# Kernel optimization log

Measured on AMD Instinct MI355X. Metric: run time of the kernel, lower is better.

## Reference

```python
import jax, jax.numpy as jnp
import numpy as np

HIDDEN = 1024
STATE = 16
EXPAND = 2
INNER = HIDDEN * EXPAND
BATCH, SEQ = 4, 2048


def setup_inputs() -> dict:
    key = jax.random.key(0)
    ks = jax.random.split(key, 12)
    s = 0.02
    return {
        "x": jax.random.normal(ks[0], (BATCH, SEQ, HIDDEN), jnp.float32),
        "norm_scale": jnp.ones((HIDDEN,), jnp.float32),
        "norm_bias": jnp.zeros((HIDDEN,), jnp.float32),
        "W_in": jax.random.normal(ks[1], (HIDDEN, 2 * INNER), jnp.float32) * s,
        "conv_w": jax.random.normal(ks[2], (INNER, 3), jnp.float32) * 0.3,
        "conv_b": jnp.zeros((INNER,), jnp.float32),
        "W_dt": jax.random.normal(ks[3], (INNER, INNER), jnp.float32) * s,
        "b_dt": jnp.zeros((INNER,), jnp.float32),
        "A_log": jax.random.normal(ks[4], (INNER, STATE), jnp.float32),
        "D_param": jnp.ones((INNER,), jnp.float32),
        "W_B": jax.random.normal(ks[5], (INNER, STATE), jnp.float32) * s,
        "W_C": jax.random.normal(ks[6], (INNER, STATE), jnp.float32) * s,
        "W_out": jax.random.normal(ks[7], (INNER, HIDDEN), jnp.float32) * s,
    }


def reference(x, norm_scale, norm_bias, W_in, conv_w, conv_b, W_dt, b_dt,
              A_log, D_param, W_B, W_C, W_out):
    residual = x
    # LayerNorm (eps = 1e-5, matches nn.LayerNorm default)
    mu = jnp.mean(x, axis=-1, keepdims=True)
    var = jnp.mean(jnp.square(x - mu), axis=-1, keepdims=True)
    xn = (x - mu) * jax.lax.rsqrt(var + 1e-5) * norm_scale + norm_bias

    xz = xn @ W_in                         # [B, L, 2*inner]
    xb, z = jnp.split(xz, 2, axis=-1)      # each [B, L, inner]

    # depthwise conv1d, kernel 3, padding 1 (cross-correlation as in torch)
    xp = jnp.pad(xb, ((0, 0), (1, 1), (0, 0)))
    xb = (conv_w[:, 0] * xp[:, :-2] + conv_w[:, 1] * xp[:, 1:-1]
          + conv_w[:, 2] * xp[:, 2:] + conv_b)
    xb = jax.nn.silu(xb)

    dt = jax.nn.softplus(xb @ W_dt + b_dt)  # [B, L, inner]
    A = -jnp.exp(A_log)                     # [inner, N]
    Bi = xb @ W_B                           # [B, L, N]
    Ci = xb @ W_C                           # [B, L, N]

    def step(h, inp):
        x_t, dt_t, B_t, C_t = inp           # [B,D], [B,D], [B,N], [B,N]
        A_bar = jnp.exp(dt_t[:, :, None] * A)                 # [B, D, N]
        h = A_bar * h + (dt_t * x_t)[:, :, None] * B_t[:, None, :]
        y_t = jnp.einsum('bdn,bn->bd', h, C_t)
        return h, y_t

    h0 = jnp.zeros((x.shape[0], INNER, STATE), x.dtype)
    xs = (jnp.swapaxes(xb, 0, 1), jnp.swapaxes(dt, 0, 1),
          jnp.swapaxes(Bi, 0, 1), jnp.swapaxes(Ci, 0, 1))
    _, y = jax.lax.scan(step, h0, xs)       # y: [L, B, D]
    y = jnp.swapaxes(y, 0, 1)

    y = (y + D_param * xb) * jax.nn.silu(z)
    return residual + y @ W_out
```

## Files before the change

kernel.cpp:

```cpp
#include <hip/hip_runtime.h>
#include <hip/hip_bf16.h>
#include <cstdint>
#include <cstddef>

#define B_DIM 4
#define L_DIM 2048
#define H_DIM 1024
#define D_DIM 2048
#define N_STATE 16
#define TOKENS (B_DIM * L_DIM)
#define CH 16
#define LC (L_DIM / CH)
#define NEXT 2176

typedef __bf16 bf16x8 __attribute__((ext_vector_type(8)));
typedef float f32x4 __attribute__((ext_vector_type(4)));

__device__ __forceinline__ float sigmoidf_(float x) { return 1.f / (1.f + __expf(-x)); }
__device__ __forceinline__ float softplusf_(float x) {
  return fmaxf(x, 0.f) + log1pf(__expf(-fabsf(x)));
}
__device__ __forceinline__ void gl_lds16(const void* g, void* l) {
  __builtin_amdgcn_global_load_lds(
      (const __attribute__((address_space(1))) unsigned int*)g,
      (__attribute__((address_space(3))) unsigned int*)l, 16, 0, 0);
}

__global__ __launch_bounds__(256) void ln_kernel(const float* __restrict__ x,
    const float* __restrict__ gamma, const float* __restrict__ beta,
    __hip_bfloat16* __restrict__ out) {
  int row = blockIdx.x;
  int t = threadIdx.x;
  const float* px = x + (size_t)row * H_DIM;
  float4 v = *(const float4*)(px + t * 4);
  float s  = v.x + v.y + v.z + v.w;
  float ss = v.x * v.x + v.y * v.y + v.z * v.z + v.w * v.w;
  for (int off = 32; off > 0; off >>= 1) {
    s  += __shfl_down(s, off);
    ss += __shfl_down(ss, off);
  }
  __shared__ float red[8];
  __shared__ float stats[2];
  int wave = t >> 6, lane = t & 63;
  if (lane == 0) { red[wave] = s; red[4 + wave] = ss; }
  __syncthreads();
  if (t == 0) {
    float S  = red[0] + red[1] + red[2] + red[3];
    float SS = red[4] + red[5] + red[6] + red[7];
    float mu = S / H_DIM;
    float var = SS / H_DIM - mu * mu;
    stats[0] = mu;
    stats[1] = rsqrtf(var + 1e-5f);
  }
  __syncthreads();
  float mu = stats[0], rstd = stats[1];
  float4 g  = *(const float4*)(gamma + t * 4);
  float4 bt = *(const float4*)(beta + t * 4);
  __hip_bfloat16* po = out + (size_t)row * H_DIM + t * 4;
  po[0] = __float2bfloat16((v.x - mu) * rstd * g.x + bt.x);
  po[1] = __float2bfloat16((v.y - mu) * rstd * g.y + bt.y);
  po[2] = __float2bfloat16((v.z - mu) * rstd * g.z + bt.z);
  po[3] = __float2bfloat16((v.w - mu) * rstd * g.w + bt.w);
}

__global__ void transpose_bf16(const float* __restrict__ in,
                               __hip_bfloat16* __restrict__ out, int R, int C) {
  __shared__ float tile[32][33];
  int c0 = blockIdx.x * 32, r0 = blockIdx.y * 32;
  int tx = threadIdx.x, ty = threadIdx.y;
  for (int i = 0; i < 32; i += 8)
    tile[ty + i][tx] = in[(size_t)(r0 + ty + i) * C + c0 + tx];
  __syncthreads();
  for (int i = 0; i < 32; i += 8)
    out[(size_t)(c0 + ty + i) * R + r0 + tx] = __float2bfloat16(tile[tx][ty + i]);
}

__global__ __launch_bounds__(256) void wbc_transpose(const float* __restrict__ WB,
    const float* __restrict__ WC, __hip_bfloat16* __restrict__ Wext) {
  int tid = blockIdx.x * 256 + threadIdx.x;
  int c = tid & 31;
  int k0 = (tid >> 5) * 16;
  const float* W = (c < 16) ? WB : WC;
  int cc = c & 15;
  __hip_bfloat16* o = Wext + (size_t)(2048 + c) * D_DIM + k0;
  for (int kk = 0; kk < 16; ++kk)
    o[kk] = __float2bfloat16(W[(size_t)(k0 + kk) * N_STATE + cc]);
}

#define BM 128
#define BN 128
#define BK 64

template <int MODE>
__global__ __launch_bounds__(256) void gemm_bf16(
    const __hip_bfloat16* __restrict__ A, const __hip_bfloat16* __restrict__ Bt,
    void* __restrict__ C0, void* __restrict__ C1, int nsplit,
    int K, int lda, int ldb, int ldc, int gx,
    const float* __restrict__ bias, const float* __restrict__ resid) {
  __shared__ __hip_bfloat16 As[BM * BK];
  __shared__ __hip_bfloat16 Bs[BN * BK];
  int t = threadIdx.x;
  int bid = blockIdx.x;
  int nsup = gx << 3;
  int super = bid / nsup;
  int rem = bid - super * nsup;
  int m0 = (super * 8 + (rem & 7)) * BM;
  int n0 = (rem >> 3) * BN;

  int wave = t >> 6, lane = t & 63;
  int quad = lane >> 4, l16 = lane & 15;
  int wm = (wave >> 1) * 64, wn = (wave & 1) * 64;

  f32x4 acc[4][4] = {};

  int srow  = t >> 3;
  int cslot = t & 7;
  int cdata = cslot ^ (srow & 7);
  const __hip_bfloat16* Ag[4];
  const __hip_bfloat16* Bg[4];
  __hip_bfloat16* Asl[4];
  __hip_bfloat16* Bsl[4];
#pragma unroll
  for (int j = 0; j < 4; ++j) {
    Ag[j]  = A  + (size_t)(m0 + j * 32 + srow) * lda + cdata * 8;
    Bg[j]  = Bt + (size_t)(n0 + j * 32 + srow) * ldb + cdata * 8;
    Asl[j] = &As[(j * 32 + srow) * BK + cslot * 8];
    Bsl[j] = &Bs[(j * 32 + srow) * BK + cslot * 8];
  }

  for (int k0 = 0; k0 < K; k0 += BK) {
    __syncthreads();
#pragma unroll
    for (int j = 0; j < 4; ++j) {
      gl_lds16(Ag[j] + k0, Asl[j]);
      gl_lds16(Bg[j] + k0, Bsl[j]);
    }
    __syncthreads();
#pragma unroll
    for (int s = 0; s < 2; ++s) {
      int cs = ((s * 4 + quad) ^ (l16 & 7)) * 8;
      bf16x8 af[4], bf_[4];
#pragma unroll
      for (int i = 0; i < 4; ++i) {
        af[i]  = *(const bf16x8*)&As[(wm + i * 16 + l16) * BK + cs];
        bf_[i] = *(const bf16x8*)&Bs[(wn + i * 16 + l16) * BK + cs];
      }
#pragma unroll
      for (int i = 0; i < 4; ++i)
#pragma unroll
        for (int j = 0; j < 4; ++j)
          acc[i][j] = __builtin_amdgcn_mfma_f32_16x16x32_bf16(af[i], bf_[j], acc[i][j], 0, 0, 0);
    }
  }

#pragma unroll
  for (int i = 0; i < 4; ++i) {
    int row0 = m0 + wm + i * 16 + quad * 4;
#pragma unroll
    for (int j = 0; j < 4; ++j) {
      int col = n0 + wn + j * 16 + l16;
      f32x4 v = acc[i][j];
      if (MODE == 0) {
#pragma unroll
        for (int r = 0; r < 4; ++r) {
          size_t idx = (size_t)(row0 + r) * ldc + col;
          ((float*)C0)[idx] = v[r] + resid[idx];
        }
      } else if (MODE == 1) {
        bool mainc = (col < nsplit);
        __hip_bfloat16* cb = mainc ? (__hip_bfloat16*)C0 : (__hip_bfloat16*)C1;
        int ccol = mainc ? col : col - nsplit;
#pragma unroll
        for (int r = 0; r < 4; ++r)
          cb[(size_t)(row0 + r) * ldc + ccol] = __float2bfloat16(v[r]);
      } else {
        if (col < nsplit) {
          float bb = bias[col];
#pragma unroll
          for (int r = 0; r < 4; ++r)
            ((__hip_bfloat16*)C0)[(size_t)(row0 + r) * ldc + col] =
                __float2bfloat16(softplusf_(v[r] + bb));
        } else {
#pragma unroll
          for (int r = 0; r < 4; ++r)
            ((float*)C1)[(size_t)(row0 + r) * 128 + (col - nsplit)] = v[r];
        }
      }
    }
  }
}

__global__ __launch_bounds__(256) void conv_silu_kernel(const __hip_bfloat16* __restrict__ xb,
    const float* __restrict__ cw, const float* __restrict__ cb,
    __hip_bfloat16* __restrict__ xbc) {
  size_t i2 = (size_t)blockIdx.x * 256 + threadIdx.x;
  int dp = (int)(i2 & (D_DIM / 2 - 1));
  size_t tok = i2 >> 10;
  int l = (int)(tok & (L_DIM - 1));
  int d = dp * 2;
  const __hip_bfloat162* base = (const __hip_bfloat162*)xb + i2;
  __hip_bfloat162 cc = base[0];
  float v0 = cw[d * 3 + 1] * __bfloat162float(cc.x) + cb[d];
  float v1 = cw[d * 3 + 4] * __bfloat162float(cc.y) + cb[d + 1];
  if (l > 0) {
    __hip_bfloat162 pm = base[-(D_DIM / 2)];
    v0 += cw[d * 3 + 0] * __bfloat162float(pm.x);
    v1 += cw[d * 3 + 3] * __bfloat162float(pm.y);
  }
  if (l < L_DIM - 1) {
    __hip_bfloat162 pp = base[D_DIM / 2];
    v0 += cw[d * 3 + 2] * __bfloat162float(pp.x);
    v1 += cw[d * 3 + 5] * __bfloat162float(pp.y);
  }
  v0 = v0 * sigmoidf_(v0);
  v1 = v1 * sigmoidf_(v1);
  __hip_bfloat162 o;
  o.x = __float2bfloat16(v0);
  o.y = __float2bfloat16(v1);
  ((__hip_bfloat162*)xbc)[i2] = o;
}

__global__ __launch_bounds__(256) void scan1_kernel(const __hip_bfloat16* __restrict__ dt,
    const __hip_bfloat16* __restrict__ xbc, const float* __restrict__ BiCi,
    const float* __restrict__ A_log, float* __restrict__ hfin,
    float* __restrict__ dtsum) {
  __shared__ float Bsh[LC * N_STATE];
  int t = threadIdx.x;
  int d = blockIdx.x * 256 + t;
  int c = blockIdx.y, b = blockIdx.z;
  size_t base = (size_t)b * L_DIM + (size_t)c * LC;
  for (int idx = t; idx < LC * 4; idx += 256) {
    int row = idx >> 2, q = idx & 3;
    ((float4*)Bsh)[row * 4 + q] = *(const float4*)&BiCi[(base + row) * 128 + q * 4];
  }
  float Aneg[N_STATE];
  {
    const float4* Ap = (const float4*)(A_log + (size_t)d * N_STATE);
#pragma unroll
    for (int q = 0; q < 4; ++q) {
      float4 av = Ap[q];
      Aneg[4 * q + 0] = -__expf(av.x);
      Aneg[4 * q + 1] = -__expf(av.y);
      Aneg[4 * q + 2] = -__expf(av.z);
      Aneg[4 * q + 3] = -__expf(av.w);
    }
  }
  __syncthreads();
  const __hip_bfloat16* dtp = dt + base * D_DIM + d;
  const __hip_bfloat16* xp = xbc + base * D_DIM + d;
  float h[N_STATE];
#pragma unroll
  for (int n = 0; n < N_STATE; ++n) h[n] = 0.f;
  float ds = 0.f;
  float dtv = __bfloat162float(dtp[0]), xv = __bfloat162float(xp[0]);
  for (int i = 0; i < LC; ++i) {
    int ip = (i < LC - 1) ? i + 1 : i;
    float dt2 = __bfloat162float(dtp[(size_t)ip * D_DIM]);
    float x2  = __bfloat162float(xp[(size_t)ip * D_DIM]);
    float dtx = dtv * xv;
    ds += dtv;
    const float4* Brow = (const float4*)&Bsh[i * N_STATE];
#pragma unroll
    for (int q = 0; q < 4; ++q) {
      float4 bv = Brow[q];
      h[4*q+0] = __expf(dtv * Aneg[4*q+0]) * h[4*q+0] + dtx * bv.x;
      h[4*q+1] = __expf(dtv * Aneg[4*q+1]) * h[4*q+1] + dtx * bv.y;
      h[4*q+2] = __expf(dtv * Aneg[4*q+2]) * h[4*q+2] + dtx * bv.z;
      h[4*q+3] = __expf(dtv * Aneg[4*q+3]) * h[4*q+3] + dtx * bv.w;
    }
    dtv = dt2; xv = x2;
  }
  float* ho = hfin + (((size_t)b * CH + c) * D_DIM + d) * N_STATE;
#pragma unroll
  for (int q = 0; q < 4; ++q) {
    float4 v; v.x = h[4*q]; v.y = h[4*q+1]; v.z = h[4*q+2]; v.w = h[4*q+3];
    ((float4*)ho)[q] = v;
  }
  dtsum[((size_t)b * CH + c) * D_DIM + d] = ds;
}

__global__ __launch_bounds__(256) void scan2_kernel(const float* __restrict__ hfin,
    const float* __restrict__ dtsum, const float* __restrict__ A_log,
    float* __restrict__ hstart) {
  int tid = blockIdx.x * 256 + threadIdx.x;
  int n = tid & 15;
  int d = (tid >> 4) & (D_DIM - 1);
  int b = tid >> 15;
  float Aneg = -__expf(A_log[d * N_STATE + n]);
  float run = 0.f;
  for (int c = 0; c < CH; ++c) {
    size_t o = (((size_t)b * CH + c) * D_DIM + d) * N_STATE + n;
    hstart[o] = run;
    run = __expf(Aneg * dtsum[((size_t)b * CH + c) * D_DIM + d]) * run + hfin[o];
  }
}

__global__ __launch_bounds__(256) void scan3_kernel(const __hip_bfloat16* __restrict__ dt,
    const __hip_bfloat16* __restrict__ xbc, const float* __restrict__ BiCi,
    const float* __restrict__ A_log,
    const float* __restrict__ hstart, const __hip_bfloat16* __restrict__ z,
    const float* __restrict__ Dp, __hip_bfloat16* __restrict__ yo) {
  __shared__ float Bsh[LC * N_STATE];
  __shared__ float Csh[LC * N_STATE];
  int t = threadIdx.x;
  int d = blockIdx.x * 256 + t;
  int c = blockIdx.y, b = blockIdx.z;
  size_t base = (size_t)b * L_DIM + (size_t)c * LC;
  for (int idx = t; idx < LC * 4; idx += 256) {
    int row = idx >> 2, q = idx & 3;
    ((float4*)Bsh)[row * 4 + q] = *(const float4*)&BiCi[(base + row) * 128 + q * 4];
    ((float4*)Csh)[row * 4 + q] = *(const float4*)&BiCi[(base + row) * 128 + 16 + q * 4];
  }
  float Aneg[N_STATE];
  {
    const float4* Ap = (const float4*)(A_log + (size_t)d * N_STATE);
#pragma unroll
    for (int q = 0; q < 4; ++q) {
      float4 av = Ap[q];
      Aneg[4 * q + 0] = -__expf(av.x);
      Aneg[4 * q + 1] = -__expf(av.y);
      Aneg[4 * q + 2] = -__expf(av.z);
      Aneg[4 * q + 3] = -__expf(av.w);
    }
  }
  float h[N_STATE];
  {
    const float4* hs = (const float4*)(hstart + (((size_t)b * CH + c) * D_DIM + d) * N_STATE);
#pragma unroll
    for (int q = 0; q < 4; ++q) {
      float4 v = hs[q];
      h[4*q] = v.x; h[4*q+1] = v.y; h[4*q+2] = v.z; h[4*q+3] = v.w;
    }
  }
  float Dv = Dp[d];
  __syncthreads();
  const __hip_bfloat16* dtp = dt + base * D_DIM + d;
  const __hip_bfloat16* xp = xbc + base * D_DIM + d;
  const __hip_bfloat16* zp = z + base * D_DIM + d;
  __hip_bfloat16* yp = yo + base * D_DIM + d;
  float dtv = __bfloat162float(dtp[0]), xv = __bfloat162float(xp[0]);
  float zv = __bfloat162float(zp[0]);
  for (int i = 0; i < LC; ++i) {
    int ip = (i < LC - 1) ? i + 1 : i;
    float dt2 = __bfloat162float(dtp[(size_t)ip * D_DIM]);
    float x2  = __bfloat162float(xp[(size_t)ip * D_DIM]);
    float z2  = __bfloat162float(zp[(size_t)ip * D_DIM]);
    float dtx = dtv * xv;
    const float4* Brow = (const float4*)&Bsh[i * N_STATE];
    const float4* Crow = (const float4*)&Csh[i * N_STATE];
    float yv = 0.f;
#pragma unroll
    for (int q = 0; q < 4; ++q) {
      float4 bv = Brow[q];
      float4 cv = Crow[q];
      h[4*q+0] = __expf(dtv * Aneg[4*q+0]) * h[4*q+0] + dtx * bv.x;
      h[4*q+1] = __expf(dtv * Aneg[4*q+1]) * h[4*q+1] + dtx * bv.y;
      h[4*q+2] = __expf(dtv * Aneg[4*q+2]) * h[4*q+2] + dtx * bv.z;
      h[4*q+3] = __expf(dtv * Aneg[4*q+3]) * h[4*q+3] + dtx * bv.w;
      yv += h[4*q+0] * cv.x + h[4*q+1] * cv.y + h[4*q+2] * cv.z + h[4*q+3] * cv.w;
    }
    float g = zv * sigmoidf_(zv);
    yp[(size_t)i * D_DIM] = __float2bfloat16((yv + Dv * xv) * g);
    dtv = dt2; xv = x2; zv = z2;
  }
}

extern "C" void kernel_launch(void* const* d_in, const int* in_sizes, int n_in,
                              void* d_out, int out_size, void* d_ws, size_t ws_size,
                              hipStream_t stream) {
  const float* x          = (const float*)d_in[0];
  const float* norm_scale = (const float*)d_in[1];
  const float* norm_bias  = (const float*)d_in[2];
  const float* W_in       = (const float*)d_in[3];
  const float* conv_w     = (const float*)d_in[4];
  const float* conv_b     = (const float*)d_in[5];
  const float* W_dt       = (const float*)d_in[6];
  const float* b_dt       = (const float*)d_in[7];
  const float* A_log      = (const float*)d_in[8];
  const float* D_param    = (const float*)d_in[9];
  const float* W_B        = (const float*)d_in[10];
  const float* W_C        = (const float*)d_in[11];
  const float* W_out      = (const float*)d_in[12];
  float* out = (float*)d_out;

  const size_t MB = 1024 * 1024;
  const size_t NEEDED = 193 * MB;
  if (ws_size < NEEDED) return;

  char* ws = (char*)d_ws;
  __hip_bfloat16* xn     = (__hip_bfloat16*)(ws);
  __hip_bfloat16* W_outT = (__hip_bfloat16*)(ws);
  float*          hfin   = (float*)(ws + 4 * MB);
  float*          dtsum  = (float*)(ws + 12 * MB);
  __hip_bfloat16* xb     = (__hip_bfloat16*)(ws + 16 * MB);
  __hip_bfloat16* ybf    = (__hip_bfloat16*)(ws + 16 * MB);
  __hip_bfloat16* z      = (__hip_bfloat16*)(ws + 48 * MB);
  __hip_bfloat16* xbc    = (__hip_bfloat16*)(ws + 80 * MB);
  __hip_bfloat16* dtY    = (__hip_bfloat16*)(ws + 112 * MB);
  float*          BiCi   = (float*)(ws + 144 * MB);
  __hip_bfloat16* W_ext  = (__hip_bfloat16*)(ws + 148 * MB);
  __hip_bfloat16* W_inT  = (__hip_bfloat16*)(ws + 177 * MB);
  float*          hstart = (float*)(ws + 177 * MB);

  dim3 tb(32, 8);
  transpose_bf16<<<dim3(4096 / 32, 1024 / 32), tb, 0, stream>>>(W_in, W_inT, 1024, 4096);
  transpose_bf16<<<dim3(2048 / 32, 2048 / 32), tb, 0, stream>>>(W_dt, W_ext, 2048, 2048);
  wbc_transpose<<<16, 256, 0, stream>>>(W_B, W_C, W_ext);
  ln_kernel<<<TOKENS, 256, 0, stream>>>(x, norm_scale, norm_bias, xn);
  gemm_bf16<1><<<(4096 / BN) * (TOKENS / BM), 256, 0, stream>>>(
      xn, W_inT, xb, z, D_DIM, H_DIM, H_DIM, H_DIM, D_DIM, 4096 / BN,
      nullptr, nullptr);
  transpose_bf16<<<dim3(1024 / 32, 2048 / 32), tb, 0, stream>>>(W_out, W_outT, 2048, 1024);
  conv_silu_kernel<<<(TOKENS * D_DIM / 2) / 256, 256, 0, stream>>>(xb, conv_w, conv_b, xbc);
  gemm_bf16<2><<<(NEXT / BN) * (TOKENS / BM), 256, 0, stream>>>(
      xbc, W_ext, dtY, BiCi, D_DIM, D_DIM, D_DIM, D_DIM, D_DIM, NEXT / BN,
      b_dt, nullptr);
  scan1_kernel<<<dim3(D_DIM / 256, CH, B_DIM), 256, 0, stream>>>(
      dtY, xbc, BiCi, A_log, hfin, dtsum);
  scan2_kernel<<<(B_DIM * D_DIM * N_STATE) / 256, 256, 0, stream>>>(
      hfin, dtsum, A_log, hstart);
  scan3_kernel<<<dim3(D_DIM / 256, CH, B_DIM), 256, 0, stream>>>(
      dtY, xbc, BiCi, A_log, hstart, z, D_param, ybf);
  gemm_bf16<0><<<(H_DIM / BN) * (TOKENS / BM), 256, 0, stream>>>(
      ybf, W_outT, out, nullptr, 1 << 30, D_DIM, D_DIM, D_DIM, H_DIM, H_DIM / BN,
      nullptr, x);
}
```

Measured before the change: 634.2 us.

## Replace 128x128 GEMM with double-buffered 256x256 tile kernel using phased MFMA scheduling

Swaps the single-buffered 128x128 bf16 GEMM for a 512-thread, 256x256-tile kernel. It double-buffers its LDS (128 KB) and prefetches the next K tiles with global-to-LDS loads while MFMAs run, split into barrier-gated phases with raised wave priority. The aim is to cut global traffic per FLOP and hide load latency behind compute in all three projection GEMMs. The dt/B/C GEMM width is padded to a multiple of 256, so it reads beyond the real weight rows and does wasted work, with the stores masked by a new column limit. The large LDS footprint also limits residency to one block per CU.

```diff
diff --git a/kernel.cpp b/kernel.cpp
--- a/kernel.cpp
+++ b/kernel.cpp
@@ -11,7 +11,8 @@
 #define TOKENS (B_DIM * L_DIM)
 #define CH 16
 #define LC (L_DIM / CH)
-#define NEXT 2176
+#define NEXT 2304
+#define NLIM2 2080
 
 typedef __bf16 bf16x8 __attribute__((ext_vector_type(8)));
 typedef float f32x4 __attribute__((ext_vector_type(4)));
@@ -87,78 +88,152 @@
     o[kk] = __float2bfloat16(W[(size_t)(k0 + kk) * N_STATE + cc]);
 }
 
-#define BM 128
-#define BN 128
-#define BK 64
-
 template <int MODE>
-__global__ __launch_bounds__(256) void gemm_bf16(
+__global__ __launch_bounds__(512, 2) void gemm256(
     const __hip_bfloat16* __restrict__ A, const __hip_bfloat16* __restrict__ Bt,
-    void* __restrict__ C0, void* __restrict__ C1, int nsplit,
-    int K, int lda, int ldb, int ldc, int gx,
+    void* __restrict__ C0, void* __restrict__ C1, int nsplit, int nlimit,
+    int K, int lda, int ldb, int ldc, int ntn,
     const float* __restrict__ bias, const float* __restrict__ resid) {
-  __shared__ __hip_bfloat16 As[BM * BK];
-  __shared__ __hip_bfloat16 Bs[BN * BK];
-  int t = threadIdx.x;
+  __shared__ __hip_bfloat16 lds[65536];
+  const int t = threadIdx.x;
+  const int nwg = gridDim.x;
   int bid = blockIdx.x;
-  int nsup = gx << 3;
-  int super = bid / nsup;
-  int rem = bid - super * nsup;
-  int m0 = (super * 8 + (rem & 7)) * BM;
-  int n0 = (rem >> 3) * BN;
-
-  int wave = t >> 6, lane = t & 63;
-  int quad = lane >> 4, l16 = lane & 15;
-  int wm = (wave >> 1) * 64, wn = (wave & 1) * 64;
-
-  f32x4 acc[4][4] = {};
-
-  int srow  = t >> 3;
-  int cslot = t & 7;
-  int cdata = cslot ^ (srow & 7);
-  const __hip_bfloat16* Ag[4];
-  const __hip_bfloat16* Bg[4];
-  __hip_bfloat16* Asl[4];
-  __hip_bfloat16* Bsl[4];
-#pragma unroll
-  for (int j = 0; j < 4; ++j) {
-    Ag[j]  = A  + (size_t)(m0 + j * 32 + srow) * lda + cdata * 8;
-    Bg[j]  = Bt + (size_t)(n0 + j * 32 + srow) * ldb + cdata * 8;
-    Asl[j] = &As[(j * 32 + srow) * BK + cslot * 8];
-    Bsl[j] = &Bs[(j * 32 + srow) * BK + cslot * 8];
-  }
-
-  for (int k0 = 0; k0 < K; k0 += BK) {
-    __syncthreads();
+  int wgid = (bid & 7) * (nwg >> 3) + (bid >> 3);
+  const int m0 = (wgid / ntn) * 256;
+  const int n0 = (wgid % ntn) * 256;
+
+  const int wave = t >> 6, lane = t & 63;
+  const int wm = wave >> 2, wn = wave & 3;
+  const int l16 = lane & 15, quad = lane >> 4;
+  const int bh = wn >> 1;
+
+  const int srow = t >> 3, cslot = t & 7;
+  const int cdata = cslot ^ (srow & 7);
+  const __hip_bfloat16* Ast = A + (size_t)(m0 + srow) * lda + cdata * 8;
+  const __hip_bfloat16* Bst = Bt + (size_t)(n0 + srow) * ldb + cdata * 8;
+  const int stoff = srow * 64 + cslot * 8;
+
+  const int ch0 = quad ^ (l16 & 7);
+  const int ch1 = ch0 ^ 4;
+  const int aoff0 = wm * 8192 + l16 * 64 + ch0 * 8;
+  const int aoff1 = wm * 8192 + l16 * 64 + ch1 * 8;
+  const int boff0 = 16384 + bh * 8192 + ((wn & 1) * 64 + l16) * 64 + ch0 * 8;
+  const int boff1 = 16384 + bh * 8192 + ((wn & 1) * 64 + l16) * 64 + ch1 * 8;
+
+  const int NT = K >> 6;
+
+#define STAGE_HT(dstb, mat, h, ktX) do {                                        \
+    const __hip_bfloat16* g_ = ((mat) ? Bst : Ast)                              \
+        + (size_t)((h) * 128) * ((mat) ? ldb : lda) + (size_t)(ktX) * 64;       \
+    __hip_bfloat16* l_ = &lds[(dstb) + (mat) * 16384 + (h) * 8192 + stoff];     \
+    gl_lds16(g_, l_);                                                           \
+    gl_lds16(g_ + (size_t)64 * ((mat) ? ldb : lda), l_ + 4096);                 \
+  } while (0)
+
+#define RD_A(aP, i0, db_) do {                                                  \
+    aP[0][0] = *(const bf16x8*)&lds[(db_) + aoff0 + (i0) * 1024];               \
+    aP[0][1] = *(const bf16x8*)&lds[(db_) + aoff1 + (i0) * 1024];               \
+    aP[1][0] = *(const bf16x8*)&lds[(db_) + aoff0 + ((i0) + 1) * 1024];         \
+    aP[1][1] = *(const bf16x8*)&lds[(db_) + aoff1 + ((i0) + 1) * 1024];         \
+  } while (0)
+
+#define RD_B(db_) do {                                                          \
+    _Pragma("unroll") for (int j = 0; j < 4; ++j) {                             \
+      bB0[j] = *(const bf16x8*)&lds[(db_) + boff0 + j * 1024];                  \
+      bB1[j] = *(const bf16x8*)&lds[(db_) + boff1 + j * 1024];                  \
+    }                                                                           \
+  } while (0)
+
+#define MFMA_PAIR(aP, i0) do {                                                  \
+    _Pragma("unroll") for (int j = 0; j < 4; ++j) {                             \
+      acc[i0][j] = __builtin_amdgcn_mfma_f32_16x16x32_bf16(                     \
+          aP[0][0], bB0[j], acc[i0][j], 0, 0, 0);                               \
+      acc[i0][j] = __builtin_amdgcn_mfma_f32_16x16x32_bf16(                     \
+          aP[0][1], bB1[j], acc[i0][j], 0, 0, 0);                               \
+      acc[(i0) + 1][j] = __builtin_amdgcn_mfma_f32_16x16x32_bf16(               \
+          aP[1][0], bB0[j], acc[(i0) + 1][j], 0, 0, 0);                         \
+      acc[(i0) + 1][j] = __builtin_amdgcn_mfma_f32_16x16x32_bf16(               \
+          aP[1][1], bB1[j], acc[(i0) + 1][j], 0, 0, 0);                         \
+    }                                                                           \
+  } while (0)
+
+#define PH_GATE() do {                                                          \
+    __builtin_amdgcn_s_barrier();                                               \
+    asm volatile("s_waitcnt lgkmcnt(0)" ::: "memory");                          \
+    __builtin_amdgcn_sched_barrier(0);                                          \
+    __builtin_amdgcn_s_setprio(1);                                              \
+  } while (0)
+
+#define PH_END() do {                                                           \
+    __builtin_amdgcn_s_setprio(0);                                              \
+    __builtin_amdgcn_sched_barrier(0);                                          \
+    __builtin_amdgcn_s_barrier();                                               \
+    asm volatile("" ::: "memory");                                              \
+    __builtin_amdgcn_sched_barrier(0);                                          \
+  } while (0)
+
+  f32x4 acc[8][4] = {};
+  bf16x8 bB0[4], bB1[4];
+  bf16x8 a01[2][2], a23[2][2], a45[2][2], a67[2][2];
+
+  STAGE_HT(0, 1, 0, 0);
+  STAGE_HT(0, 1, 1, 0);
+  STAGE_HT(0, 0, 0, 0);
+  STAGE_HT(0, 0, 1, 0);
+  STAGE_HT(32768, 1, 0, 1);
+  STAGE_HT(32768, 1, 1, 1);
+  STAGE_HT(32768, 0, 0, 1);
+  asm volatile("s_waitcnt vmcnt(6)" ::: "memory");
+  __builtin_amdgcn_s_barrier();
+  asm volatile("" ::: "memory");
+
+  for (int kt = 0; kt < NT; ++kt) {
+    const int db32 = (kt & 1) << 15;
+    const int dn32 = db32 ^ 32768;
+    const bool p1 = (kt + 1 < NT);
+    const bool p2 = (kt + 2 < NT);
+    RD_B(db32);
+    RD_A(a01, 0, db32);
+    if (p1) STAGE_HT(dn32, 0, 1, kt + 1);
+    PH_GATE();
+    MFMA_PAIR(a01, 0);
+    PH_END();
+    RD_A(a23, 2, db32);
+    RD_A(a45, 4, db32);
+    if (p2) STAGE_HT(db32, 1, 0, kt + 2);
+    PH_GATE();
+    MFMA_PAIR(a23, 2);
+    PH_END();
+    RD_A(a67, 6, db32);
+    if (p2) STAGE_HT(db32, 1, 1, kt + 2);
+    PH_GATE();
+    MFMA_PAIR(a45, 4);
+    PH_END();
+    if (p2) STAGE_HT(db32, 0, 0, kt + 2);
+    __builtin_amdgcn_s_barrier();
+    __builtin_amdgcn_sched_barrier(0);
+    __builtin_amdgcn_s_setprio(1);
+    MFMA_PAIR(a67, 6);
+    __builtin_amdgcn_s_setprio(0);
+    __builtin_amdgcn_sched_barrier(0);
+    if (p2) {
+      asm volatile("s_waitcnt vmcnt(6)" ::: "memory");
+    } else {
+      asm volatile("s_waitcnt vmcnt(0)" ::: "memory");
+    }
+    __builtin_amdgcn_s_barrier();
+    asm volatile("" ::: "memory");
+    __builtin_amdgcn_sched_barrier(0);
+  }
+
+  const int row_base = m0 + wm * 128;
+  const int col_base = n0 + wn * 64;
+#pragma unroll
+  for (int i = 0; i < 8; ++i) {
+    const int row0 = row_base + i * 16 + quad * 4;
 #pragma unroll
     for (int j = 0; j < 4; ++j) {
-      gl_lds16(Ag[j] + k0, Asl[j]);
-      gl_lds16(Bg[j] + k0, Bsl[j]);
-    }
-    __syncthreads();
-#pragma unroll
-    for (int s = 0; s < 2; ++s) {
-      int cs = ((s * 4 + quad) ^ (l16 & 7)) * 8;
-      bf16x8 af[4], bf_[4];
-#pragma unroll
-      for (int i = 0; i < 4; ++i) {
-        af[i]  = *(const bf16x8*)&As[(wm + i * 16 + l16) * BK + cs];
-        bf_[i] = *(const bf16x8*)&Bs[(wn + i * 16 + l16) * BK + cs];
-      }
-#pragma unroll
-      for (int i = 0; i < 4; ++i)
-#pragma unroll
-        for (int j = 0; j < 4; ++j)
-          acc[i][j] = __builtin_amdgcn_mfma_f32_16x16x32_bf16(af[i], bf_[j], acc[i][j], 0, 0, 0);
-    }
-  }
-
-#pragma unroll
-  for (int i = 0; i < 4; ++i) {
-    int row0 = m0 + wm + i * 16 + quad * 4;
-#pragma unroll
-    for (int j = 0; j < 4; ++j) {
-      int col = n0 + wn + j * 16 + l16;
+      const int col = col_base + j * 16 + l16;
       f32x4 v = acc[i][j];
       if (MODE == 0) {
 #pragma unroll
@@ -180,7 +255,7 @@
           for (int r = 0; r < 4; ++r)
             ((__hip_bfloat16*)C0)[(size_t)(row0 + r) * ldc + col] =
                 __float2bfloat16(softplusf_(v[r] + bb));
-        } else {
+        } else if (col < nlimit) {
 #pragma unroll
           for (int r = 0; r < 4; ++r)
             ((float*)C1)[(size_t)(row0 + r) * 128 + (col - nsplit)] = v[r];
@@ -188,6 +263,12 @@
       }
     }
   }
+#undef STAGE_HT
+#undef RD_A
+#undef RD_B
+#undef MFMA_PAIR
+#undef PH_GATE
+#undef PH_END
 }
 
 __global__ __launch_bounds__(256) void conv_silu_kernel(const __hip_bfloat16* __restrict__ xb,
@@ -407,13 +488,13 @@
   transpose_bf16<<<dim3(2048 / 32, 2048 / 32), tb, 0, stream>>>(W_dt, W_ext, 2048, 2048);
   wbc_transpose<<<16, 256, 0, stream>>>(W_B, W_C, W_ext);
   ln_kernel<<<TOKENS, 256, 0, stream>>>(x, norm_scale, norm_bias, xn);
-  gemm_bf16<1><<<(4096 / BN) * (TOKENS / BM), 256, 0, stream>>>(
-      xn, W_inT, xb, z, D_DIM, H_DIM, H_DIM, H_DIM, D_DIM, 4096 / BN,
+  gemm256<1><<<(TOKENS / 256) * (4096 / 256), 512, 0, stream>>>(
+      xn, W_inT, xb, z, D_DIM, 1 << 30, H_DIM, H_DIM, H_DIM, D_DIM, 4096 / 256,
       nullptr, nullptr);
   transpose_bf16<<<dim3(1024 / 32, 2048 / 32), tb, 0, stream>>>(W_out, W_outT, 2048, 1024);
   conv_silu_kernel<<<(TOKENS * D_DIM / 2) / 256, 256, 0, stream>>>(xb, conv_w, conv_b, xbc);
-  gemm_bf16<2><<<(NEXT / BN) * (TOKENS / BM), 256, 0, stream>>>(
-      xbc, W_ext, dtY, BiCi, D_DIM, D_DIM, D_DIM, D_DIM, D_DIM, NEXT / BN,
+  gemm256<2><<<(TOKENS / 256) * (NEXT / 256), 512, 0, stream>>>(
+      xbc, W_ext, dtY, BiCi, D_DIM, NLIM2, D_DIM, D_DIM, D_DIM, D_DIM, NEXT / 256,
       b_dt, nullptr);
   scan1_kernel<<<dim3(D_DIM / 256, CH, B_DIM), 256, 0, stream>>>(
       dtY, xbc, BiCi, A_log, hfin, dtsum);
@@ -421,7 +502,7 @@
       hfin, dtsum, A_log, hstart);
   scan3_kernel<<<dim3(D_DIM / 256, CH, B_DIM), 256, 0, stream>>>(
       dtY, xbc, BiCi, A_log, hstart, z, D_param, ybf);
-  gemm_bf16<0><<<(H_DIM / BN) * (TOKENS / BM), 256, 0, stream>>>(
-      ybf, W_outT, out, nullptr, 1 << 30, D_DIM, D_DIM, D_DIM, H_DIM, H_DIM / BN,
-      nullptr, x);
-}
+  gemm256<0><<<(TOKENS / 256) * (1024 / 256), 512, 0, stream>>>(
+      ybf, W_outT, out, nullptr, 1 << 30, 1 << 30, D_DIM, D_DIM, D_DIM, H_DIM,
+      1024 / 256, nullptr, x);
+}
```

Measured after the change: 671.3 us. +5.8%, slower.

## Double-buffer GEMM LDS tiles and double scan chunk count

Applied to the files above, without the earlier changes.

The bf16 GEMM now keeps two LDS buffers and issues the global-to-LDS loads for the next K tile before computing on the current one, so load latency overlaps with MFMA work and one barrier per iteration is dropped. Separately, the scan chunk count rises from 16 to 32 for more parallelism in the chunked scan, and the workspace buffers for hfin, dtsum and hstart are moved to fit the larger chunk state. Double buffering doubles LDS use to 64KB per block, which may reduce occupancy.

```diff
diff --git a/kernel.cpp b/kernel.cpp
--- a/kernel.cpp
+++ b/kernel.cpp
@@ -9,7 +9,7 @@
 #define D_DIM 2048
 #define N_STATE 16
 #define TOKENS (B_DIM * L_DIM)
-#define CH 16
+#define CH 32
 #define LC (L_DIM / CH)
 #define NEXT 2176
 
@@ -97,8 +97,8 @@
     void* __restrict__ C0, void* __restrict__ C1, int nsplit,
     int K, int lda, int ldb, int ldc, int gx,
     const float* __restrict__ bias, const float* __restrict__ resid) {
-  __shared__ __hip_bfloat16 As[BM * BK];
-  __shared__ __hip_bfloat16 Bs[BN * BK];
+  __shared__ __hip_bfloat16 As[2 * BM * BK];
+  __shared__ __hip_bfloat16 Bs[2 * BN * BK];
   int t = threadIdx.x;
   int bid = blockIdx.x;
   int nsup = gx << 3;
@@ -118,32 +118,42 @@
   int cdata = cslot ^ (srow & 7);
   const __hip_bfloat16* Ag[4];
   const __hip_bfloat16* Bg[4];
-  __hip_bfloat16* Asl[4];
-  __hip_bfloat16* Bsl[4];
+  int soff[4];
 #pragma unroll
   for (int j = 0; j < 4; ++j) {
     Ag[j]  = A  + (size_t)(m0 + j * 32 + srow) * lda + cdata * 8;
     Bg[j]  = Bt + (size_t)(n0 + j * 32 + srow) * ldb + cdata * 8;
-    Asl[j] = &As[(j * 32 + srow) * BK + cslot * 8];
-    Bsl[j] = &Bs[(j * 32 + srow) * BK + cslot * 8];
-  }
-
-  for (int k0 = 0; k0 < K; k0 += BK) {
-    __syncthreads();
-#pragma unroll
-    for (int j = 0; j < 4; ++j) {
-      gl_lds16(Ag[j] + k0, Asl[j]);
-      gl_lds16(Bg[j] + k0, Bsl[j]);
-    }
-    __syncthreads();
+    soff[j] = (j * 32 + srow) * BK + cslot * 8;
+  }
+
+  const int NT = K / BK;
+#pragma unroll
+  for (int j = 0; j < 4; ++j) {
+    gl_lds16(Ag[j], &As[soff[j]]);
+    gl_lds16(Bg[j], &Bs[soff[j]]);
+  }
+  asm volatile("s_waitcnt vmcnt(0)" ::: "memory");
+  __builtin_amdgcn_s_barrier();
+
+  for (int kt = 0; kt < NT; ++kt) {
+    const int cur = (kt & 1) * (BM * BK);
+    const int nxt = cur ^ (BM * BK);
+    if (kt + 1 < NT) {
+      const int k1 = (kt + 1) * BK;
+#pragma unroll
+      for (int j = 0; j < 4; ++j) {
+        gl_lds16(Ag[j] + k1, &As[nxt + soff[j]]);
+        gl_lds16(Bg[j] + k1, &Bs[nxt + soff[j]]);
+      }
+    }
 #pragma unroll
     for (int s = 0; s < 2; ++s) {
       int cs = ((s * 4 + quad) ^ (l16 & 7)) * 8;
       bf16x8 af[4], bf_[4];
 #pragma unroll
       for (int i = 0; i < 4; ++i) {
-        af[i]  = *(const bf16x8*)&As[(wm + i * 16 + l16) * BK + cs];
-        bf_[i] = *(const bf16x8*)&Bs[(wn + i * 16 + l16) * BK + cs];
+        af[i]  = *(const bf16x8*)&As[cur + (wm + i * 16 + l16) * BK + cs];
+        bf_[i] = *(const bf16x8*)&Bs[cur + (wn + i * 16 + l16) * BK + cs];
       }
 #pragma unroll
       for (int i = 0; i < 4; ++i)
@@ -151,6 +161,8 @@
         for (int j = 0; j < 4; ++j)
           acc[i][j] = __builtin_amdgcn_mfma_f32_16x16x32_bf16(af[i], bf_[j], acc[i][j], 0, 0, 0);
     }
+    asm volatile("s_waitcnt vmcnt(0)" ::: "memory");
+    __builtin_amdgcn_s_barrier();
   }
 
 #pragma unroll
@@ -390,8 +402,6 @@
   char* ws = (char*)d_ws;
   __hip_bfloat16* xn     = (__hip_bfloat16*)(ws);
   __hip_bfloat16* W_outT = (__hip_bfloat16*)(ws);
-  float*          hfin   = (float*)(ws + 4 * MB);
-  float*          dtsum  = (float*)(ws + 12 * MB);
   __hip_bfloat16* xb     = (__hip_bfloat16*)(ws + 16 * MB);
   __hip_bfloat16* ybf    = (__hip_bfloat16*)(ws + 16 * MB);
   __hip_bfloat16* z      = (__hip_bfloat16*)(ws + 48 * MB);
@@ -399,8 +409,10 @@
   __hip_bfloat16* dtY    = (__hip_bfloat16*)(ws + 112 * MB);
   float*          BiCi   = (float*)(ws + 144 * MB);
   __hip_bfloat16* W_ext  = (__hip_bfloat16*)(ws + 148 * MB);
+  float*          hstart = (float*)(ws + 158 * MB);
+  float*          dtsum  = (float*)(ws + 174 * MB);
   __hip_bfloat16* W_inT  = (__hip_bfloat16*)(ws + 177 * MB);
-  float*          hstart = (float*)(ws + 177 * MB);
+  float*          hfin   = (float*)(ws + 177 * MB);
 
   dim3 tb(32, 8);
   transpose_bf16<<<dim3(4096 / 32, 1024 / 32), tb, 0, stream>>>(W_in, W_inT, 1024, 4096);
```

New measurement: 575.5 us. -9.3%, faster.
